# Kernel tuning notes

Hardware: AMD Instinct MI355X
Metric: run time of the kernel (lower is better)

Reference implementation:

```python
import jax, jax.numpy as jnp
import numpy as np

B, S, H = 2, 256, 768
LR = 0.01
EPS = 1e-5  # torch LayerNorm default


def setup_inputs() -> dict:
    key = jax.random.key(0)
    ks = jax.random.split(key, 6)
    f = jnp.float32
    return {
        "x": jax.random.normal(ks[0], (B, S, H), f),
        "W_init": jax.random.normal(ks[1], (H, H), f) * 0.02,
        "b_init": jnp.zeros((H,), f),
        "gate_w": jax.random.normal(ks[2], (4 * H, H), f) * 0.02,
        "gate_b": jnp.zeros((4 * H,), f),
        "up_w": jax.random.normal(ks[3], (4 * H, H), f) * 0.02,
        "up_b": jnp.zeros((4 * H,), f),
        "down_w": jax.random.normal(ks[4], (H, 4 * H), f) * 0.02,
        "down_b": jnp.zeros((H,), f),
        "norm_w": jnp.ones((H,), f),
        "norm_b": jnp.zeros((H,), f),
    }


def _layernorm(x, w, b):
    mu = jnp.mean(x, axis=-1, keepdims=True)
    var = jnp.var(x, axis=-1, keepdims=True)
    return (x - mu) * jax.lax.rsqrt(var + EPS) * w + b


def reference(x, W_init, b_init, gate_w, gate_b, up_w, up_b,
              down_w, down_b, norm_w, norm_b):
    # x: [B, S, H]. Sequential TTT fast-weight recurrence, vectorized over batch,
    # scanned over time (equivalent to the per-token Python loop in torch).
    Bn, Sn, Hn = x.shape
    xs = jnp.swapaxes(x, 0, 1)                                   # [S, B, H]
    x_next = jnp.concatenate([xs[1:], jnp.zeros_like(xs[:1])], 0)  # target x[t+1]
    # lr per step; the update is skipped at the last token (t == S-1)
    lr = jnp.concatenate([jnp.full((Sn - 1,), LR, x.dtype),
                          jnp.zeros((1,), x.dtype)])

    W0 = jnp.broadcast_to(W_init, (Bn, Hn, Hn))
    b0 = jnp.broadcast_to(b_init, (Bn, Hn))

    def step(carry, inp):
        W, b = carry
        xt, xn, lr_t = inp
        pred = jnp.einsum('bij,bj->bi', W, xt) + b               # fast-weight matvec
        gated = jax.nn.sigmoid(pred @ gate_w.T + gate_b) * (pred @ up_w.T + up_b)
        out = _layernorm(gated @ down_w.T + down_b + pred, norm_w, norm_b)
        diff = pred - xn                                         # prediction error
        W = W - lr_t * diff[:, :, None] * xt[:, None, :]         # rank-1 update
        b = b - lr_t * diff
        return (W, b), out

    _, ys = jax.lax.scan(step, (W0, b0), (xs, x_next, lr))       # ys: [S, B, H]
    return jnp.swapaxes(ys, 0, 1)
```

## Files before the change

kernel.cpp:

```cpp
#include <hip/hip_runtime.h>
#include <hip/hip_bf16.h>

#define H   768
#define H4  3072
#define S   256
#define BB  2
#define M   (BB * S)
#define LRC 0.01f
#define C   64
#define NC  (S / C)

typedef __attribute__((ext_vector_type(8))) short bf16x8;
typedef __attribute__((ext_vector_type(4))) float f32x4;

__device__ inline short bfbits(float f) {
    __hip_bfloat16 h = __float2bfloat16(f);
    return *reinterpret_cast<short*>(&h);
}

__global__ __launch_bounds__(256) void k_stage(
    const float* __restrict__ x,  const float* __restrict__ W0,
    const float* __restrict__ gw, const float* __restrict__ uw,
    const float* __restrict__ dw,
    short* __restrict__ Xhi, short* __restrict__ Xlo,
    short* __restrict__ Whi, short* __restrict__ Wlo,
    short* __restrict__ gw2, short* __restrict__ uw2, short* __restrict__ dw2)
{
    const long gid = (long)blockIdx.x * 256 + threadIdx.x;
    const float* src; short* hp; short* lp = nullptr; long base;
    if (gid < 98304)        { src = x;  hp = Xhi; lp = Xlo; base = 0; }
    else if (gid < 245760)  { src = W0; hp = Whi; lp = Wlo; base = 98304; }
    else if (gid < 835584)  { src = gw; hp = gw2; base = 245760; }
    else if (gid < 1425408) { src = uw; hp = uw2; base = 835584; }
    else                    { src = dw; hp = dw2; base = 1425408; }
    const long i = (gid - base) * 4;
    const float4 v = *(const float4*)(src + i);
    const float vf[4] = {v.x, v.y, v.z, v.w};
    short h4[4], l4[4];
#pragma unroll
    for (int j = 0; j < 4; ++j) {
        h4[j] = bfbits(vf[j]);
        __hip_bfloat16 hb = *reinterpret_cast<__hip_bfloat16*>(&h4[j]);
        l4[j] = bfbits(vf[j] - __bfloat162float(hb));
    }
    *(uint2*)(hp + i) = *(uint2*)h4;
    if (lp) *(uint2*)(lp + i) = *(uint2*)l4;
}

__global__ __launch_bounds__(256) void k_gram_base(
    const short* __restrict__ Xhi, const short* __restrict__ Xlo,
    const short* __restrict__ Whi, const short* __restrict__ Wlo,
    const float* __restrict__ b0,
    float* __restrict__ g, float* __restrict__ base0)
{
    const int wid = threadIdx.x >> 6, lane = threadIdx.x & 63;
    const int r16 = lane & 15, quad = lane >> 4;
    const int id = blockIdx.x;

    f32x4 acc[4];
#pragma unroll
    for (int i = 0; i < 4; ++i) acc[i] = (f32x4){0, 0, 0, 0};

    if (id < 32) {
        const int bx = id & 3, by = (id >> 2) & 3, b = id >> 4;
        const int m0 = by * 64, n0 = bx * 64 + wid * 16;
        const short* XH = Xhi + b * S * H;
        const short* XL = Xlo + b * S * H;
        for (int k0 = 0; k0 < H; k0 += 32) {
            const int k = k0 + quad * 8;
            const bf16x8 bh = *(const bf16x8*)(XH + (n0 + r16) * H + k);
            const bf16x8 bl = *(const bf16x8*)(XL + (n0 + r16) * H + k);
#pragma unroll
            for (int i = 0; i < 4; ++i) {
                const bf16x8 ah = *(const bf16x8*)(XH + (m0 + i * 16 + r16) * H + k);
                const bf16x8 al = *(const bf16x8*)(XL + (m0 + i * 16 + r16) * H + k);
                acc[i] = __builtin_amdgcn_mfma_f32_16x16x32_bf16(ah, bh, acc[i], 0, 0, 0);
                acc[i] = __builtin_amdgcn_mfma_f32_16x16x32_bf16(ah, bl, acc[i], 0, 0, 0);
                acc[i] = __builtin_amdgcn_mfma_f32_16x16x32_bf16(al, bh, acc[i], 0, 0, 0);
            }
        }
        const int col = n0 + r16;
#pragma unroll
        for (int i = 0; i < 4; ++i)
#pragma unroll
            for (int r = 0; r < 4; ++r) {
                const int row = m0 + i * 16 + quad * 4 + r;
                g[(b * S + row) * S + col] = acc[i][r] + 1.f;
            }
    } else {
        const int id2 = id - 32;
        const int m0 = (id2 / 12) * 64, n0 = (id2 % 12) * 64 + wid * 16;
        for (int k0 = 0; k0 < H; k0 += 32) {
            const int k = k0 + quad * 8;
            const bf16x8 bh = *(const bf16x8*)(Whi + (n0 + r16) * H + k);
            const bf16x8 bl = *(const bf16x8*)(Wlo + (n0 + r16) * H + k);
#pragma unroll
            for (int i = 0; i < 4; ++i) {
                const bf16x8 ah = *(const bf16x8*)(Xhi + (m0 + i * 16 + r16) * H + k);
                const bf16x8 al = *(const bf16x8*)(Xlo + (m0 + i * 16 + r16) * H + k);
                acc[i] = __builtin_amdgcn_mfma_f32_16x16x32_bf16(ah, bh, acc[i], 0, 0, 0);
                acc[i] = __builtin_amdgcn_mfma_f32_16x16x32_bf16(ah, bl, acc[i], 0, 0, 0);
                acc[i] = __builtin_amdgcn_mfma_f32_16x16x32_bf16(al, bh, acc[i], 0, 0, 0);
            }
        }
        const int col = n0 + r16;
        const float bv = b0[col];
#pragma unroll
        for (int i = 0; i < 4; ++i)
#pragma unroll
            for (int r = 0; r < 4; ++r) {
                const int row = m0 + i * 16 + quad * 4 + r;
                base0[row * H + col] = acc[i][r] + bv;
            }
    }
}

__global__ __launch_bounds__(256) void k_recur3(
    const float* __restrict__ x,
    const float* __restrict__ base0,
    const float* __restrict__ g,
    float* __restrict__ pred_f,
    __hip_bfloat16* __restrict__ pred_h)
{
    __shared__ float tB[64 * 17];
    __shared__ float tX[64 * 17];
    __shared__ float Dl[256 * 17];
    __shared__ float Gs[64 * 65];
    const int tid = threadIdx.x;
    const int w = tid >> 6, lane = tid & 63;
    const int b = blockIdx.x / 48, hb = blockIdx.x % 48;
    const int h0 = hb * 16;
    const int ho = w * 4;
    const int ct = tid >> 2;
    const int cq = (tid & 3) * 4;

    for (int c = 0; c < NC; ++c) {
        const int t0 = c * C;
        __syncthreads();
        {
            const int gm = b * S + t0 + ct;
            const float4 bv = *(const float4*)(base0 + gm * H + h0 + cq);
            float4 xv = {0.f, 0.f, 0.f, 0.f};
            if (t0 + ct + 1 < S)
                xv = *(const float4*)(x + (gm + 1) * H + h0 + cq);
            tB[ct * 17 + cq + 0] = bv.x - xv.x;
            tB[ct * 17 + cq + 1] = bv.y - xv.y;
            tB[ct * 17 + cq + 2] = bv.z - xv.z;
            tB[ct * 17 + cq + 3] = bv.w - xv.w;
            tX[ct * 17 + cq + 0] = xv.x;
            tX[ct * 17 + cq + 1] = xv.y;
            tX[ct * 17 + cq + 2] = xv.z;
            tX[ct * 17 + cq + 3] = xv.w;
#pragma unroll
            for (int j = 0; j < 16; ++j) {
                const int idx = tid + 256 * j;
                const int row = idx >> 6, col = idx & 63;
                Gs[row * 65 + col] = g[(long)(b * S + t0 + row) * S + t0 + col];
            }
        }
        __syncthreads();
        float R[4], Xn[4];
#pragma unroll
        for (int h = 0; h < 4; ++h) {
            R[h]  = tB[lane * 17 + ho + h];
            Xn[h] = tX[lane * 17 + ho + h];
        }
        const float* gcol = g + (long)(b * S) * S + t0 + lane;
#pragma unroll 4
        for (int cs = 0; cs < t0; ++cs) {
            const float Gv = gcol[(long)cs * S];
            const float* dr = &Dl[cs * 17 + ho];
            R[0] -= LRC * Gv * dr[0];
            R[1] -= LRC * Gv * dr[1];
            R[2] -= LRC * Gv * dr[2];
            R[3] -= LRC * Gv * dr[3];
        }
        for (int s = 0; s < C; ++s) {
            float dsb[4];
#pragma unroll
            for (int h = 0; h < 4; ++h) dsb[h] = __shfl(R[h], s, 64);
            const float Gv = Gs[s * 65 + lane];
            const float mlt = (lane > s) ? LRC : 0.f;
#pragma unroll
            for (int h = 0; h < 4; ++h) R[h] -= mlt * Gv * dsb[h];
        }
#pragma unroll
        for (int h = 0; h < 4; ++h) Dl[(t0 + lane) * 17 + ho + h] = R[h];
        __syncthreads();
#pragma unroll
        for (int h = 0; h < 4; ++h) tB[lane * 17 + ho + h] = R[h] + Xn[h];
        __syncthreads();
        {
            const int gm = b * S + t0 + ct;
            float4 pv;
            pv.x = tB[ct * 17 + cq + 0];
            pv.y = tB[ct * 17 + cq + 1];
            pv.z = tB[ct * 17 + cq + 2];
            pv.w = tB[ct * 17 + cq + 3];
            *(float4*)(pred_f + gm * H + h0 + cq) = pv;
            short p4[4];
            p4[0] = bfbits(pv.x); p4[1] = bfbits(pv.y);
            p4[2] = bfbits(pv.z); p4[3] = bfbits(pv.w);
            *(uint2*)((short*)pred_h + gm * H + h0 + cq) = *(uint2*)p4;
        }
    }
}

#define RS 40
__global__ __launch_bounds__(256) void k_gateup3(
    const __hip_bfloat16* __restrict__ predh,
    const short* __restrict__ gwp, const float* __restrict__ gb,
    const short* __restrict__ uwp, const float* __restrict__ ub,
    __hip_bfloat16* __restrict__ hid)
{
    __shared__ int4 smv[1600];
    short* sm = (short*)smv;
    short* sA = sm;
    short* sG = sm + 64 * RS;
    short* sU = sm + (64 + 128) * RS;

    const int tid = threadIdx.x;
    const int wid = tid >> 6, lane = tid & 63;
    const int r16 = lane & 15, quad = lane >> 4;
    const int wm = wid & 1, wn = wid >> 1;
    const int n0 = blockIdx.x * 128;
    const int m0 = blockIdx.y * 64;

    const int srow = tid >> 2;
    const int sch  = (tid & 3) * 8;
    const short* A = (const short*)predh;

    f32x4 ag[2][4], au[2][4];
#pragma unroll
    for (int i = 0; i < 2; ++i)
#pragma unroll
        for (int j = 0; j < 4; ++j) { ag[i][j] = (f32x4){0,0,0,0}; au[i][j] = (f32x4){0,0,0,0}; }

    int4 rA, rG0, rG1, rU0, rU1;
    {
        const int k = sch;
        rA  = *(const int4*)(A   + (m0 + srow) * H + k);
        rG0 = *(const int4*)(gwp + (n0 + srow) * H + k);
        rG1 = *(const int4*)(gwp + (n0 + 64 + srow) * H + k);
        rU0 = *(const int4*)(uwp + (n0 + srow) * H + k);
        rU1 = *(const int4*)(uwp + (n0 + 64 + srow) * H + k);
    }
    for (int it = 0; it < 24; ++it) {
        *(int4*)(sA + srow * RS + sch)        = rA;
        *(int4*)(sG + srow * RS + sch)        = rG0;
        *(int4*)(sG + (64 + srow) * RS + sch) = rG1;
        *(int4*)(sU + srow * RS + sch)        = rU0;
        *(int4*)(sU + (64 + srow) * RS + sch) = rU1;
        __syncthreads();
        if (it < 23) {
            const int k = (it + 1) * 32 + sch;
            rA  = *(const int4*)(A   + (m0 + srow) * H + k);
            rG0 = *(const int4*)(gwp + (n0 + srow) * H + k);
            rG1 = *(const int4*)(gwp + (n0 + 64 + srow) * H + k);
            rU0 = *(const int4*)(uwp + (n0 + srow) * H + k);
            rU1 = *(const int4*)(uwp + (n0 + 64 + srow) * H + k);
        }
        bf16x8 aF[2], gF[4], uF[4];
#pragma unroll
        for (int i = 0; i < 2; ++i)
            aF[i] = *(const bf16x8*)(sA + (wm * 32 + i * 16 + r16) * RS + quad * 8);
#pragma unroll
        for (int j = 0; j < 4; ++j) {
            gF[j] = *(const bf16x8*)(sG + (wn * 64 + j * 16 + r16) * RS + quad * 8);
            uF[j] = *(const bf16x8*)(sU + (wn * 64 + j * 16 + r16) * RS + quad * 8);
        }
#pragma unroll
        for (int i = 0; i < 2; ++i)
#pragma unroll
            for (int j = 0; j < 4; ++j) {
                ag[i][j] = __builtin_amdgcn_mfma_f32_16x16x32_bf16(aF[i], gF[j], ag[i][j], 0, 0, 0);
                au[i][j] = __builtin_amdgcn_mfma_f32_16x16x32_bf16(aF[i], uF[j], au[i][j], 0, 0, 0);
            }
        __syncthreads();
    }
#pragma unroll
    for (int j = 0; j < 4; ++j) {
        const int ocol = n0 + wn * 64 + j * 16 + r16;
        const float gbv = gb[ocol], ubv = ub[ocol];
#pragma unroll
        for (int i = 0; i < 2; ++i)
#pragma unroll
            for (int r = 0; r < 4; ++r) {
                const int orow = m0 + wm * 32 + i * 16 + quad * 4 + r;
                const float gg = ag[i][j][r] + gbv;
                const float u  = au[i][j][r] + ubv;
                const float sg = 1.f / (1.f + __expf(-gg));
                hid[orow * H4 + ocol] = __float2bfloat16(sg * u);
            }
    }
}

__device__ inline bf16x8 ldb32(const void* p, long off) {
    const float* f = (const float*)p + off;
    const float4 a = *(const float4*)f;
    const float4 b = *(const float4*)(f + 4);
    bf16x8 r;
    r[0] = bfbits(a.x); r[1] = bfbits(a.y); r[2] = bfbits(a.z); r[3] = bfbits(a.w);
    r[4] = bfbits(b.x); r[5] = bfbits(b.y); r[6] = bfbits(b.z); r[7] = bfbits(b.w);
    return r;
}
__device__ inline bf16x8 ldb16(const void* p, long off) {
    return *(const bf16x8*)((const short*)p + off);
}

template<bool WB>
__global__ __launch_bounds__(256) void k_gateup2(
    const __hip_bfloat16* __restrict__ predh,
    const void* __restrict__ gw, const float* __restrict__ gb,
    const void* __restrict__ uw, const float* __restrict__ ub,
    __hip_bfloat16* __restrict__ hid)
{
    const int wid = threadIdx.x >> 6, lane = threadIdx.x & 63;
    const int r16 = lane & 15, quad = lane >> 4;
    const int m0 = blockIdx.y * 64;
    const int n0 = blockIdx.x * 64 + wid * 16;

    f32x4 ag[4], au[4];
#pragma unroll
    for (int i = 0; i < 4; ++i) { ag[i] = (f32x4){0,0,0,0}; au[i] = (f32x4){0,0,0,0}; }
    const short* A = (const short*)predh;
    const long brow = (long)(n0 + r16) * H;

    for (int k0 = 0; k0 < H; k0 += 32) {
        const int k = k0 + quad * 8;
        const bf16x8 bg = WB ? ldb16(gw, brow + k) : ldb32(gw, brow + k);
        const bf16x8 bu = WB ? ldb16(uw, brow + k) : ldb32(uw, brow + k);
#pragma unroll
        for (int i = 0; i < 4; ++i) {
            const bf16x8 af = *(const bf16x8*)(A + (m0 + i * 16 + r16) * H + k);
            ag[i] = __builtin_amdgcn_mfma_f32_16x16x32_bf16(af, bg, ag[i], 0, 0, 0);
            au[i] = __builtin_amdgcn_mfma_f32_16x16x32_bf16(af, bu, au[i], 0, 0, 0);
        }
    }
    const int ocol = n0 + r16;
    const float gbv = gb[ocol], ubv = ub[ocol];
#pragma unroll
    for (int i = 0; i < 4; ++i)
#pragma unroll
        for (int r = 0; r < 4; ++r) {
            const int orow = m0 + i * 16 + quad * 4 + r;
            const float gg = ag[i][r] + gbv;
            const float u = au[i][r] + ubv;
            const float sg = 1.f / (1.f + __expf(-gg));
            hid[orow * H4 + ocol] = __float2bfloat16(sg * u);
        }
}

template<bool WB>
__global__ __launch_bounds__(256) void k_down2(
    const __hip_bfloat16* __restrict__ hid,
    const void* __restrict__ dw, const float* __restrict__ db,
    const float* __restrict__ predf, float* __restrict__ dout)
{
    const int wid = threadIdx.x >> 6, lane = threadIdx.x & 63;
    const int r16 = lane & 15, quad = lane >> 4;
    const int m0 = blockIdx.y * 32;
    const int n0 = blockIdx.x * 64 + wid * 16;

    f32x4 ac[2];
    ac[0] = (f32x4){0,0,0,0}; ac[1] = (f32x4){0,0,0,0};
    const short* A = (const short*)hid;
    const long brow = (long)(n0 + r16) * H4;

    for (int k0 = 0; k0 < H4; k0 += 32) {
        const int k = k0 + quad * 8;
        const bf16x8 bd = WB ? ldb16(dw, brow + k) : ldb32(dw, brow + k);
#pragma unroll
        for (int i = 0; i < 2; ++i) {
            const bf16x8 af = *(const bf16x8*)(A + (m0 + i * 16 + r16) * H4 + k);
            ac[i] = __builtin_amdgcn_mfma_f32_16x16x32_bf16(af, bd, ac[i], 0, 0, 0);
        }
    }
    const int ocol = n0 + r16;
    const float dbv = db[ocol];
#pragma unroll
    for (int i = 0; i < 2; ++i)
#pragma unroll
        for (int r = 0; r < 4; ++r) {
            const int orow = m0 + i * 16 + quad * 4 + r;
            dout[orow * H + ocol] = ac[i][r] + dbv + predf[orow * H + ocol];
        }
}

__global__ __launch_bounds__(256) void k_ln(
    const float* __restrict__ dout,
    const float* __restrict__ nw,
    const float* __restrict__ nb,
    float* __restrict__ out)
{
    const int m = blockIdx.x;
    const int tid = threadIdx.x;
    const float* rowp = dout + m * H;

    float v[3];
    float s = 0.f, s2 = 0.f;
#pragma unroll
    for (int j = 0; j < 3; ++j) {
        v[j] = rowp[tid + 256 * j];
        s += v[j];
        s2 += v[j] * v[j];
    }
#pragma unroll
    for (int off = 32; off >= 1; off >>= 1) {
        s  += __shfl_xor(s, off, 64);
        s2 += __shfl_xor(s2, off, 64);
    }
    __shared__ float rs[4], rs2[4];
    const int wid = tid >> 6, lane = tid & 63;
    if (lane == 0) { rs[wid] = s; rs2[wid] = s2; }
    __syncthreads();
    s  = rs[0] + rs[1] + rs[2] + rs[3];
    s2 = rs2[0] + rs2[1] + rs2[2] + rs2[3];
    const float mu  = s / (float)H;
    const float var = s2 / (float)H - mu * mu;
    const float inv = rsqrtf(var + 1e-5f);
#pragma unroll
    for (int j = 0; j < 3; ++j) {
        const int hh = tid + 256 * j;
        out[m * H + hh] = (v[j] - mu) * inv * nw[hh] + nb[hh];
    }
}

extern "C" void kernel_launch(void* const* d_in, const int* in_sizes, int n_in,
                              void* d_out, int out_size, void* d_ws, size_t ws_size,
                              hipStream_t stream)
{
    const float* x   = (const float*)d_in[0];
    const float* W0  = (const float*)d_in[1];
    const float* b0  = (const float*)d_in[2];
    const float* gw  = (const float*)d_in[3];
    const float* gb  = (const float*)d_in[4];
    const float* uw  = (const float*)d_in[5];
    const float* ub  = (const float*)d_in[6];
    const float* dw  = (const float*)d_in[7];
    const float* db  = (const float*)d_in[8];
    const float* nw  = (const float*)d_in[9];
    const float* nb  = (const float*)d_in[10];

    char* ws = (char*)d_ws;
    float*          pred_f = (float*)(ws);
    __hip_bfloat16* pred_h = (__hip_bfloat16*)(ws + 1572864);
    __hip_bfloat16* hid    = (__hip_bfloat16*)(ws + 2359296);
    float*          base0  = (float*)(ws + 5505024);
    float*          dout_f = (float*)(ws + 5505024);
    float*          g      = (float*)(ws + 7077888);
    short*          Xhi    = (short*)(ws + 7602176);
    short*          Xlo    = (short*)(ws + 8388608);
    short*          Whi    = (short*)(ws + 9175040);
    short*          Wlo    = (short*)(ws + 10354688);
    const size_t WNEED = 11534336ULL + 3ULL * 4718592ULL;
    const bool wb = ws_size >= WNEED;
    short* gw2 = (short*)(ws + 11534336);
    short* uw2 = (short*)(ws + 11534336 + 4718592);
    short* dw2 = (short*)(ws + 11534336 + 2 * 4718592);

    const int ngroups = wb ? 2015232 : 245760;
    k_stage<<<dim3(ngroups / 256), 256, 0, stream>>>(
        x, W0, gw, uw, dw, Xhi, Xlo, Whi, Wlo, gw2, uw2, dw2);
    k_gram_base<<<dim3(128), 256, 0, stream>>>(Xhi, Xlo, Whi, Wlo, b0, g, base0);
    k_recur3<<<dim3(96), 256, 0, stream>>>(x, base0, g, pred_f, pred_h);
    if (wb) {
        k_gateup3<<<dim3(H4 / 128, M / 64), 256, 0, stream>>>(pred_h, gw2, gb, uw2, ub, hid);
        k_down2<true><<<dim3(H / 64, M / 32), 256, 0, stream>>>(hid, dw2, db, pred_f, dout_f);
    } else {
        k_gateup2<false><<<dim3(H4 / 64, M / 64), 256, 0, stream>>>(pred_h, gw, gb, uw, ub, hid);
        k_down2<false><<<dim3(H / 64, M / 32), 256, 0, stream>>>(hid, dw, db, pred_f, dout_f);
    }
    k_ln<<<dim3(M), 256, 0, stream>>>(dout_f, nw, nb, (float*)d_out);
}
```

Baseline: 227.3 us.

## Fuse all stages into one cooperative persistent megakernel with grid syncs

Replaces the six separate kernel launches with a single cooperative kernel of 256 workgroups. The stages (weight staging, Gram/base GEMMs, recurrence, gate/up, down, layernorm) run in sequence, separated by grid.sync(). It also adds a precomputed per-chunk intra-chunk solve matrix U, computed in parallel, and re-splits the recurrence across 192 workgroups instead of 96. The aim is to remove launch gaps and raise parallelism in the serial recurrence. In exchange it adds grid-wide barrier costs, limits occupancy to one block per CU, and drops the fallback path for a small workspace.

```diff
diff --git a/kernel.cpp b/kernel.cpp
--- a/kernel.cpp
+++ b/kernel.cpp
@@ -1,5 +1,8 @@
 #include <hip/hip_runtime.h>
 #include <hip/hip_bf16.h>
+#include <hip/hip_cooperative_groups.h>
+
+namespace cg = cooperative_groups;
 
 #define H   768
 #define H4  3072
@@ -9,6 +12,8 @@
 #define LRC 0.01f
 #define C   64
 #define NC  (S / C)
+#define RS  40
+#define RS2 72
 
 typedef __attribute__((ext_vector_type(8))) short bf16x8;
 typedef __attribute__((ext_vector_type(4))) float f32x4;
@@ -18,411 +23,385 @@
     return *reinterpret_cast<short*>(&h);
 }
 
-__global__ __launch_bounds__(256) void k_stage(
+struct RecSM {
+    float2 Dl2[1024];
+    float2 Rl2[256];
+    float  tB[576];
+    float  tX[576];
+    float  Us[4160];
+    float  Gslab[12288];
+};
+union alignas(16) SM {
+    RecSM rec;
+    struct { short sA[64 * RS]; short sG[128 * RS]; short sU[128 * RS]; } gu;
+    struct { short sA[32 * RS2]; short sB[64 * RS2]; } dn;
+    float Gi[4160];
+    struct { float rs[4]; float rs2[4]; } ln;
+};
+
+__global__ void __launch_bounds__(256, 1) k_mega(
     const float* __restrict__ x,  const float* __restrict__ W0,
-    const float* __restrict__ gw, const float* __restrict__ uw,
-    const float* __restrict__ dw,
+    const float* __restrict__ b0,
+    const float* __restrict__ gw, const float* __restrict__ gb,
+    const float* __restrict__ uw, const float* __restrict__ ub,
+    const float* __restrict__ dw, const float* __restrict__ db,
+    const float* __restrict__ nw, const float* __restrict__ nb,
     short* __restrict__ Xhi, short* __restrict__ Xlo,
     short* __restrict__ Whi, short* __restrict__ Wlo,
-    short* __restrict__ gw2, short* __restrict__ uw2, short* __restrict__ dw2)
+    short* __restrict__ gw2, short* __restrict__ uw2, short* __restrict__ dw2,
+    float* __restrict__ g, float* __restrict__ base0, float* __restrict__ U,
+    float* __restrict__ pred_f, __hip_bfloat16* __restrict__ pred_h,
+    __hip_bfloat16* __restrict__ hid,
+    float* __restrict__ dout_f, float* __restrict__ out)
 {
-    const long gid = (long)blockIdx.x * 256 + threadIdx.x;
-    const float* src; short* hp; short* lp = nullptr; long base;
-    if (gid < 98304)        { src = x;  hp = Xhi; lp = Xlo; base = 0; }
-    else if (gid < 245760)  { src = W0; hp = Whi; lp = Wlo; base = 98304; }
-    else if (gid < 835584)  { src = gw; hp = gw2; base = 245760; }
-    else if (gid < 1425408) { src = uw; hp = uw2; base = 835584; }
-    else                    { src = dw; hp = dw2; base = 1425408; }
-    const long i = (gid - base) * 4;
-    const float4 v = *(const float4*)(src + i);
-    const float vf[4] = {v.x, v.y, v.z, v.w};
-    short h4[4], l4[4];
-#pragma unroll
-    for (int j = 0; j < 4; ++j) {
-        h4[j] = bfbits(vf[j]);
-        __hip_bfloat16 hb = *reinterpret_cast<__hip_bfloat16*>(&h4[j]);
-        l4[j] = bfbits(vf[j] - __bfloat162float(hb));
-    }
-    *(uint2*)(hp + i) = *(uint2*)h4;
-    if (lp) *(uint2*)(lp + i) = *(uint2*)l4;
-}
-
-__global__ __launch_bounds__(256) void k_gram_base(
-    const short* __restrict__ Xhi, const short* __restrict__ Xlo,
-    const short* __restrict__ Whi, const short* __restrict__ Wlo,
-    const float* __restrict__ b0,
-    float* __restrict__ g, float* __restrict__ base0)
-{
-    const int wid = threadIdx.x >> 6, lane = threadIdx.x & 63;
-    const int r16 = lane & 15, quad = lane >> 4;
-    const int id = blockIdx.x;
-
-    f32x4 acc[4];
-#pragma unroll
-    for (int i = 0; i < 4; ++i) acc[i] = (f32x4){0, 0, 0, 0};
-
-    if (id < 32) {
-        const int bx = id & 3, by = (id >> 2) & 3, b = id >> 4;
-        const int m0 = by * 64, n0 = bx * 64 + wid * 16;
-        const short* XH = Xhi + b * S * H;
-        const short* XL = Xlo + b * S * H;
-        for (int k0 = 0; k0 < H; k0 += 32) {
-            const int k = k0 + quad * 8;
-            const bf16x8 bh = *(const bf16x8*)(XH + (n0 + r16) * H + k);
-            const bf16x8 bl = *(const bf16x8*)(XL + (n0 + r16) * H + k);
-#pragma unroll
-            for (int i = 0; i < 4; ++i) {
-                const bf16x8 ah = *(const bf16x8*)(XH + (m0 + i * 16 + r16) * H + k);
-                const bf16x8 al = *(const bf16x8*)(XL + (m0 + i * 16 + r16) * H + k);
-                acc[i] = __builtin_amdgcn_mfma_f32_16x16x32_bf16(ah, bh, acc[i], 0, 0, 0);
-                acc[i] = __builtin_amdgcn_mfma_f32_16x16x32_bf16(ah, bl, acc[i], 0, 0, 0);
-                acc[i] = __builtin_amdgcn_mfma_f32_16x16x32_bf16(al, bh, acc[i], 0, 0, 0);
-            }
-        }
-        const int col = n0 + r16;
-#pragma unroll
-        for (int i = 0; i < 4; ++i)
-#pragma unroll
-            for (int r = 0; r < 4; ++r) {
-                const int row = m0 + i * 16 + quad * 4 + r;
-                g[(b * S + row) * S + col] = acc[i][r] + 1.f;
-            }
-    } else {
-        const int id2 = id - 32;
-        const int m0 = (id2 / 12) * 64, n0 = (id2 % 12) * 64 + wid * 16;
-        for (int k0 = 0; k0 < H; k0 += 32) {
-            const int k = k0 + quad * 8;
-            const bf16x8 bh = *(const bf16x8*)(Whi + (n0 + r16) * H + k);
-            const bf16x8 bl = *(const bf16x8*)(Wlo + (n0 + r16) * H + k);
-#pragma unroll
-            for (int i = 0; i < 4; ++i) {
-                const bf16x8 ah = *(const bf16x8*)(Xhi + (m0 + i * 16 + r16) * H + k);
-                const bf16x8 al = *(const bf16x8*)(Xlo + (m0 + i * 16 + r16) * H + k);
-                acc[i] = __builtin_amdgcn_mfma_f32_16x16x32_bf16(ah, bh, acc[i], 0, 0, 0);
-                acc[i] = __builtin_amdgcn_mfma_f32_16x16x32_bf16(ah, bl, acc[i], 0, 0, 0);
-                acc[i] = __builtin_amdgcn_mfma_f32_16x16x32_bf16(al, bh, acc[i], 0, 0, 0);
-            }
-        }
-        const int col = n0 + r16;
-        const float bv = b0[col];
-#pragma unroll
-        for (int i = 0; i < 4; ++i)
-#pragma unroll
-            for (int r = 0; r < 4; ++r) {
-                const int row = m0 + i * 16 + quad * 4 + r;
-                base0[row * H + col] = acc[i][r] + bv;
-            }
-    }
-}
-
-__global__ __launch_bounds__(256) void k_recur3(
-    const float* __restrict__ x,
-    const float* __restrict__ base0,
-    const float* __restrict__ g,
-    float* __restrict__ pred_f,
-    __hip_bfloat16* __restrict__ pred_h)
-{
-    __shared__ float tB[64 * 17];
-    __shared__ float tX[64 * 17];
-    __shared__ float Dl[256 * 17];
-    __shared__ float Gs[64 * 65];
+    __shared__ SM sm;
+    cg::grid_group grid = cg::this_grid();
     const int tid = threadIdx.x;
-    const int w = tid >> 6, lane = tid & 63;
-    const int b = blockIdx.x / 48, hb = blockIdx.x % 48;
-    const int h0 = hb * 16;
-    const int ho = w * 4;
-    const int ct = tid >> 2;
-    const int cq = (tid & 3) * 4;
-
-    for (int c = 0; c < NC; ++c) {
-        const int t0 = c * C;
-        __syncthreads();
-        {
-            const int gm = b * S + t0 + ct;
-            const float4 bv = *(const float4*)(base0 + gm * H + h0 + cq);
-            float4 xv = {0.f, 0.f, 0.f, 0.f};
-            if (t0 + ct + 1 < S)
-                xv = *(const float4*)(x + (gm + 1) * H + h0 + cq);
-            tB[ct * 17 + cq + 0] = bv.x - xv.x;
-            tB[ct * 17 + cq + 1] = bv.y - xv.y;
-            tB[ct * 17 + cq + 2] = bv.z - xv.z;
-            tB[ct * 17 + cq + 3] = bv.w - xv.w;
-            tX[ct * 17 + cq + 0] = xv.x;
-            tX[ct * 17 + cq + 1] = xv.y;
-            tX[ct * 17 + cq + 2] = xv.z;
-            tX[ct * 17 + cq + 3] = xv.w;
-#pragma unroll
-            for (int j = 0; j < 16; ++j) {
-                const int idx = tid + 256 * j;
-                const int row = idx >> 6, col = idx & 63;
-                Gs[row * 65 + col] = g[(long)(b * S + t0 + row) * S + t0 + col];
-            }
-        }
-        __syncthreads();
-        float R[4], Xn[4];
-#pragma unroll
-        for (int h = 0; h < 4; ++h) {
-            R[h]  = tB[lane * 17 + ho + h];
-            Xn[h] = tX[lane * 17 + ho + h];
-        }
-        const float* gcol = g + (long)(b * S) * S + t0 + lane;
-#pragma unroll 4
-        for (int cs = 0; cs < t0; ++cs) {
-            const float Gv = gcol[(long)cs * S];
-            const float* dr = &Dl[cs * 17 + ho];
-            R[0] -= LRC * Gv * dr[0];
-            R[1] -= LRC * Gv * dr[1];
-            R[2] -= LRC * Gv * dr[2];
-            R[3] -= LRC * Gv * dr[3];
-        }
-        for (int s = 0; s < C; ++s) {
-            float dsb[4];
-#pragma unroll
-            for (int h = 0; h < 4; ++h) dsb[h] = __shfl(R[h], s, 64);
-            const float Gv = Gs[s * 65 + lane];
-            const float mlt = (lane > s) ? LRC : 0.f;
-#pragma unroll
-            for (int h = 0; h < 4; ++h) R[h] -= mlt * Gv * dsb[h];
-        }
-#pragma unroll
-        for (int h = 0; h < 4; ++h) Dl[(t0 + lane) * 17 + ho + h] = R[h];
-        __syncthreads();
-#pragma unroll
-        for (int h = 0; h < 4; ++h) tB[lane * 17 + ho + h] = R[h] + Xn[h];
-        __syncthreads();
-        {
-            const int gm = b * S + t0 + ct;
-            float4 pv;
-            pv.x = tB[ct * 17 + cq + 0];
-            pv.y = tB[ct * 17 + cq + 1];
-            pv.z = tB[ct * 17 + cq + 2];
-            pv.w = tB[ct * 17 + cq + 3];
-            *(float4*)(pred_f + gm * H + h0 + cq) = pv;
-            short p4[4];
-            p4[0] = bfbits(pv.x); p4[1] = bfbits(pv.y);
-            p4[2] = bfbits(pv.z); p4[3] = bfbits(pv.w);
-            *(uint2*)((short*)pred_h + gm * H + h0 + cq) = *(uint2*)p4;
-        }
-    }
-}
-
-#define RS 40
-__global__ __launch_bounds__(256) void k_gateup3(
-    const __hip_bfloat16* __restrict__ predh,
-    const short* __restrict__ gwp, const float* __restrict__ gb,
-    const short* __restrict__ uwp, const float* __restrict__ ub,
-    __hip_bfloat16* __restrict__ hid)
-{
-    __shared__ int4 smv[1600];
-    short* sm = (short*)smv;
-    short* sA = sm;
-    short* sG = sm + 64 * RS;
-    short* sU = sm + (64 + 128) * RS;
-
-    const int tid = threadIdx.x;
+    const int wg  = blockIdx.x;
     const int wid = tid >> 6, lane = tid & 63;
     const int r16 = lane & 15, quad = lane >> 4;
-    const int wm = wid & 1, wn = wid >> 1;
-    const int n0 = blockIdx.x * 128;
-    const int m0 = blockIdx.y * 64;
-
-    const int srow = tid >> 2;
-    const int sch  = (tid & 3) * 8;
-    const short* A = (const short*)predh;
-
-    f32x4 ag[2][4], au[2][4];
-#pragma unroll
-    for (int i = 0; i < 2; ++i)
-#pragma unroll
-        for (int j = 0; j < 4; ++j) { ag[i][j] = (f32x4){0,0,0,0}; au[i][j] = (f32x4){0,0,0,0}; }
-
-    int4 rA, rG0, rG1, rU0, rU1;
+
+    for (long gid = (long)wg * 256 + tid; gid < 2015232; gid += 65536) {
+        const float* src; short* hp; short* lp = nullptr; long base;
+        if (gid < 98304)        { src = x;  hp = Xhi; lp = Xlo; base = 0; }
+        else if (gid < 245760)  { src = W0; hp = Whi; lp = Wlo; base = 98304; }
+        else if (gid < 835584)  { src = gw; hp = gw2; base = 245760; }
+        else if (gid < 1425408) { src = uw; hp = uw2; base = 835584; }
+        else                    { src = dw; hp = dw2; base = 1425408; }
+        const long i = (gid - base) * 4;
+        const float4 v = *(const float4*)(src + i);
+        const float vf[4] = {v.x, v.y, v.z, v.w};
+        short h4[4], l4[4];
+#pragma unroll
+        for (int j = 0; j < 4; ++j) {
+            h4[j] = bfbits(vf[j]);
+            __hip_bfloat16 hb = *reinterpret_cast<__hip_bfloat16*>(&h4[j]);
+            l4[j] = bfbits(vf[j] - __bfloat162float(hb));
+        }
+        *(uint2*)(hp + i) = *(uint2*)h4;
+        if (lp) *(uint2*)(lp + i) = *(uint2*)l4;
+    }
+    grid.sync();
+
     {
-        const int k = sch;
-        rA  = *(const int4*)(A   + (m0 + srow) * H + k);
-        rG0 = *(const int4*)(gwp + (n0 + srow) * H + k);
-        rG1 = *(const int4*)(gwp + (n0 + 64 + srow) * H + k);
-        rU0 = *(const int4*)(uwp + (n0 + srow) * H + k);
-        rU1 = *(const int4*)(uwp + (n0 + 64 + srow) * H + k);
-    }
-    for (int it = 0; it < 24; ++it) {
-        *(int4*)(sA + srow * RS + sch)        = rA;
-        *(int4*)(sG + srow * RS + sch)        = rG0;
-        *(int4*)(sG + (64 + srow) * RS + sch) = rG1;
-        *(int4*)(sU + srow * RS + sch)        = rU0;
-        *(int4*)(sU + (64 + srow) * RS + sch) = rU1;
+        f32x4 acc[2];
+        acc[0] = (f32x4){0, 0, 0, 0};
+        acc[1] = (f32x4){0, 0, 0, 0};
+        if (wg < 64) {
+            const int bx = wg & 3, by = (wg >> 2) & 7, b = wg >> 5;
+            const int m0 = by * 32, n0 = bx * 64 + wid * 16;
+            const short* XH = Xhi + b * S * H;
+            const short* XL = Xlo + b * S * H;
+            for (int k0 = 0; k0 < H; k0 += 32) {
+                const int k = k0 + quad * 8;
+                const bf16x8 bh = *(const bf16x8*)(XH + (n0 + r16) * H + k);
+                const bf16x8 bl = *(const bf16x8*)(XL + (n0 + r16) * H + k);
+#pragma unroll
+                for (int i = 0; i < 2; ++i) {
+                    const bf16x8 ah = *(const bf16x8*)(XH + (m0 + i * 16 + r16) * H + k);
+                    const bf16x8 al = *(const bf16x8*)(XL + (m0 + i * 16 + r16) * H + k);
+                    acc[i] = __builtin_amdgcn_mfma_f32_16x16x32_bf16(ah, bh, acc[i], 0, 0, 0);
+                    acc[i] = __builtin_amdgcn_mfma_f32_16x16x32_bf16(ah, bl, acc[i], 0, 0, 0);
+                    acc[i] = __builtin_amdgcn_mfma_f32_16x16x32_bf16(al, bh, acc[i], 0, 0, 0);
+                }
+            }
+            const int col = n0 + r16;
+#pragma unroll
+            for (int i = 0; i < 2; ++i)
+#pragma unroll
+                for (int r = 0; r < 4; ++r) {
+                    const int row = m0 + i * 16 + quad * 4 + r;
+                    g[(b * S + row) * S + col] = acc[i][r] + 1.f;
+                }
+        } else {
+            const int id2 = wg - 64;
+            const int m0 = (id2 / 12) * 32, n0 = (id2 % 12) * 64 + wid * 16;
+            for (int k0 = 0; k0 < H; k0 += 32) {
+                const int k = k0 + quad * 8;
+                const bf16x8 bh = *(const bf16x8*)(Whi + (n0 + r16) * H + k);
+                const bf16x8 bl = *(const bf16x8*)(Wlo + (n0 + r16) * H + k);
+#pragma unroll
+                for (int i = 0; i < 2; ++i) {
+                    const bf16x8 ah = *(const bf16x8*)(Xhi + (m0 + i * 16 + r16) * H + k);
+                    const bf16x8 al = *(const bf16x8*)(Xlo + (m0 + i * 16 + r16) * H + k);
+                    acc[i] = __builtin_amdgcn_mfma_f32_16x16x32_bf16(ah, bh, acc[i], 0, 0, 0);
+                    acc[i] = __builtin_amdgcn_mfma_f32_16x16x32_bf16(ah, bl, acc[i], 0, 0, 0);
+                    acc[i] = __builtin_amdgcn_mfma_f32_16x16x32_bf16(al, bh, acc[i], 0, 0, 0);
+                }
+            }
+            const int col = n0 + r16;
+            const float bv = b0[col];
+#pragma unroll
+            for (int i = 0; i < 2; ++i)
+#pragma unroll
+                for (int r = 0; r < 4; ++r) {
+                    const int row = m0 + i * 16 + quad * 4 + r;
+                    base0[row * H + col] = acc[i][r] + bv;
+                }
+        }
+    }
+    grid.sync();
+
+    if (wg < BB * NC) {
+        const int b = wg >> 2, c = wg & 3;
+        const int t0 = c * C;
+#pragma unroll
+        for (int j = 0; j < 16; ++j) {
+            const int idx = tid + 256 * j;
+            const int row = idx >> 6, col = idx & 63;
+            sm.Gi[row * 65 + col] = g[(long)(b * S + t0 + row) * S + t0 + col];
+        }
         __syncthreads();
-        if (it < 23) {
-            const int k = (it + 1) * 32 + sch;
-            rA  = *(const int4*)(A   + (m0 + srow) * H + k);
-            rG0 = *(const int4*)(gwp + (n0 + srow) * H + k);
-            rG1 = *(const int4*)(gwp + (n0 + 64 + srow) * H + k);
-            rU0 = *(const int4*)(uwp + (n0 + srow) * H + k);
-            rU1 = *(const int4*)(uwp + (n0 + 64 + srow) * H + k);
-        }
-        bf16x8 aF[2], gF[4], uF[4];
+        const int j0 = wid * 16;
+        float R[16];
+#pragma unroll
+        for (int i = 0; i < 16; ++i) R[i] = (lane == j0 + i) ? 1.f : 0.f;
+        for (int s = 0; s < C - 1; ++s) {
+            const float Gv = sm.Gi[s * 65 + lane];
+            const float mlt = (lane > s) ? LRC : 0.f;
+#pragma unroll
+            for (int i = 0; i < 16; ++i) {
+                const float dsb = __shfl(R[i], s, 64);
+                R[i] -= mlt * Gv * dsb;
+            }
+        }
+        float* Ub = U + (long)(b * NC + c) * C * C;
+#pragma unroll
+        for (int i = 0; i < 16; ++i)
+            Ub[lane * C + j0 + i] = R[i];
+    }
+    grid.sync();
+
+    if (wg < 192) {
+        const int b = wg / 96, hb = wg % 96;
+        const int h0 = hb * 8;
+        const int ho = wid * 2;
+        const int ct = tid >> 2;
+        const int cq = (tid & 3) * 2;
+        for (int c = 0; c < NC; ++c) {
+            const int t0 = c * C;
+            __syncthreads();
+            {
+                const int gm = b * S + t0 + ct;
+                const float2 bv = *(const float2*)(base0 + gm * H + h0 + cq);
+                float2 xv = {0.f, 0.f};
+                if (t0 + ct + 1 < S)
+                    xv = *(const float2*)(x + (gm + 1) * H + h0 + cq);
+                sm.rec.tB[ct * 9 + cq + 0] = bv.x - xv.x;
+                sm.rec.tB[ct * 9 + cq + 1] = bv.y - xv.y;
+                sm.rec.tX[ct * 9 + cq + 0] = xv.x;
+                sm.rec.tX[ct * 9 + cq + 1] = xv.y;
+                const float* Ub = U + (long)(b * NC + c) * C * C;
+#pragma unroll
+                for (int j = 0; j < 16; ++j) {
+                    const int idx = tid + 256 * j;
+                    const int row = idx >> 6, col = idx & 63;
+                    sm.rec.Us[row * 65 + col] = Ub[row * C + col];
+                }
+                const float* gb2 = g + (long)(b * S) * S + t0;
+                for (int i = tid; i < t0 * 64; i += 256) {
+                    const int row = i >> 6, col = i & 63;
+                    sm.rec.Gslab[i] = gb2[(long)row * S + col];
+                }
+            }
+            __syncthreads();
+            float R[2], Xn[2];
+#pragma unroll
+            for (int h = 0; h < 2; ++h) {
+                R[h]  = sm.rec.tB[lane * 9 + ho + h];
+                Xn[h] = sm.rec.tX[lane * 9 + ho + h];
+            }
+#pragma unroll 8
+            for (int cs = 0; cs < t0; ++cs) {
+                const float Gv = sm.rec.Gslab[cs * 64 + lane];
+                const float2 dr = sm.rec.Dl2[cs * 4 + wid];
+                R[0] -= LRC * Gv * dr.x;
+                R[1] -= LRC * Gv * dr.y;
+            }
+            sm.rec.Rl2[wid * 64 + lane] = (float2){R[0], R[1]};
+            float D[2] = {0.f, 0.f};
+#pragma unroll 8
+            for (int s = 0; s < C; ++s) {
+                const float2 rb = sm.rec.Rl2[wid * 64 + s];
+                const float uv = sm.rec.Us[lane * 65 + s];
+                D[0] += uv * rb.x;
+                D[1] += uv * rb.y;
+            }
+            sm.rec.Dl2[(t0 + lane) * 4 + wid] = (float2){D[0], D[1]};
+            __syncthreads();
+#pragma unroll
+            for (int h = 0; h < 2; ++h) sm.rec.tB[lane * 9 + ho + h] = D[h] + Xn[h];
+            __syncthreads();
+            {
+                const int gm = b * S + t0 + ct;
+                float2 pv;
+                pv.x = sm.rec.tB[ct * 9 + cq + 0];
+                pv.y = sm.rec.tB[ct * 9 + cq + 1];
+                *(float2*)(pred_f + gm * H + h0 + cq) = pv;
+                short p2[2];
+                p2[0] = bfbits(pv.x); p2[1] = bfbits(pv.y);
+                *(unsigned int*)((short*)pred_h + gm * H + h0 + cq) = *(unsigned int*)p2;
+            }
+        }
+    }
+    grid.sync();
+
+    if (wg < 192) {
+        const int n0 = (wg % 24) * 128;
+        const int m0 = (wg / 24) * 64;
+        const int wm = wid & 1, wn = wid >> 1;
+        const int srow = tid >> 2;
+        const int sch  = (tid & 3) * 8;
+        const short* A = (const short*)pred_h;
+
+        f32x4 ag[2][4], au[2][4];
 #pragma unroll
         for (int i = 0; i < 2; ++i)
-            aF[i] = *(const bf16x8*)(sA + (wm * 32 + i * 16 + r16) * RS + quad * 8);
+#pragma unroll
+            for (int j = 0; j < 4; ++j) { ag[i][j] = (f32x4){0,0,0,0}; au[i][j] = (f32x4){0,0,0,0}; }
+
+        int4 rA, rG0, rG1, rU0, rU1;
+        rA  = *(const int4*)(A   + (m0 + srow) * H + sch);
+        rG0 = *(const int4*)(gw2 + (n0 + srow) * H + sch);
+        rG1 = *(const int4*)(gw2 + (n0 + 64 + srow) * H + sch);
+        rU0 = *(const int4*)(uw2 + (n0 + srow) * H + sch);
+        rU1 = *(const int4*)(uw2 + (n0 + 64 + srow) * H + sch);
+        for (int it = 0; it < 24; ++it) {
+            *(int4*)(sm.gu.sA + srow * RS + sch)        = rA;
+            *(int4*)(sm.gu.sG + srow * RS + sch)        = rG0;
+            *(int4*)(sm.gu.sG + (64 + srow) * RS + sch) = rG1;
+            *(int4*)(sm.gu.sU + srow * RS + sch)        = rU0;
+            *(int4*)(sm.gu.sU + (64 + srow) * RS + sch) = rU1;
+            __syncthreads();
+            if (it < 23) {
+                const int k = (it + 1) * 32 + sch;
+                rA  = *(const int4*)(A   + (m0 + srow) * H + k);
+                rG0 = *(const int4*)(gw2 + (n0 + srow) * H + k);
+                rG1 = *(const int4*)(gw2 + (n0 + 64 + srow) * H + k);
+                rU0 = *(const int4*)(uw2 + (n0 + srow) * H + k);
+                rU1 = *(const int4*)(uw2 + (n0 + 64 + srow) * H + k);
+            }
+            bf16x8 aF[2], gF[4], uF[4];
+#pragma unroll
+            for (int i = 0; i < 2; ++i)
+                aF[i] = *(const bf16x8*)(sm.gu.sA + (wm * 32 + i * 16 + r16) * RS + quad * 8);
+#pragma unroll
+            for (int j = 0; j < 4; ++j) {
+                gF[j] = *(const bf16x8*)(sm.gu.sG + (wn * 64 + j * 16 + r16) * RS + quad * 8);
+                uF[j] = *(const bf16x8*)(sm.gu.sU + (wn * 64 + j * 16 + r16) * RS + quad * 8);
+            }
+#pragma unroll
+            for (int i = 0; i < 2; ++i)
+#pragma unroll
+                for (int j = 0; j < 4; ++j) {
+                    ag[i][j] = __builtin_amdgcn_mfma_f32_16x16x32_bf16(aF[i], gF[j], ag[i][j], 0, 0, 0);
+                    au[i][j] = __builtin_amdgcn_mfma_f32_16x16x32_bf16(aF[i], uF[j], au[i][j], 0, 0, 0);
+                }
+            __syncthreads();
+        }
 #pragma unroll
         for (int j = 0; j < 4; ++j) {
-            gF[j] = *(const bf16x8*)(sG + (wn * 64 + j * 16 + r16) * RS + quad * 8);
-            uF[j] = *(const bf16x8*)(sU + (wn * 64 + j * 16 + r16) * RS + quad * 8);
-        }
-#pragma unroll
-        for (int i = 0; i < 2; ++i)
-#pragma unroll
-            for (int j = 0; j < 4; ++j) {
-                ag[i][j] = __builtin_amdgcn_mfma_f32_16x16x32_bf16(aF[i], gF[j], ag[i][j], 0, 0, 0);
-                au[i][j] = __builtin_amdgcn_mfma_f32_16x16x32_bf16(aF[i], uF[j], au[i][j], 0, 0, 0);
-            }
+            const int ocol = n0 + wn * 64 + j * 16 + r16;
+            const float gbv = gb[ocol], ubv = ub[ocol];
+#pragma unroll
+            for (int i = 0; i < 2; ++i)
+#pragma unroll
+                for (int r = 0; r < 4; ++r) {
+                    const int orow = m0 + wm * 32 + i * 16 + quad * 4 + r;
+                    const float gg = ag[i][j][r] + gbv;
+                    const float u  = au[i][j][r] + ubv;
+                    const float sg = 1.f / (1.f + __expf(-gg));
+                    hid[orow * H4 + ocol] = __float2bfloat16(sg * u);
+                }
+        }
+    }
+    grid.sync();
+
+    if (wg < 192) {
+        const int n0 = (wg % 12) * 64;
+        const int m0 = (wg / 12) * 32;
+        const int wm = wid & 1, wn = wid >> 1;
+        const short* A = (const short*)hid;
+
+        f32x4 ac[2];
+        ac[0] = (f32x4){0,0,0,0}; ac[1] = (f32x4){0,0,0,0};
+
+        const int arow = tid >> 3, ach = (tid & 7) * 8;
+        const int brow1 = arow + 32;
+
+        int4 rA, rB0, rB1;
+        rA  = *(const int4*)(A   + (m0 + arow) * H4 + ach);
+        rB0 = *(const int4*)(dw2 + (n0 + arow) * H4 + ach);
+        rB1 = *(const int4*)(dw2 + (n0 + brow1) * H4 + ach);
+        for (int it = 0; it < 48; ++it) {
+            *(int4*)(sm.dn.sA + arow * RS2 + ach)  = rA;
+            *(int4*)(sm.dn.sB + arow * RS2 + ach)  = rB0;
+            *(int4*)(sm.dn.sB + brow1 * RS2 + ach) = rB1;
+            __syncthreads();
+            if (it < 47) {
+                const int k = (it + 1) * 64 + ach;
+                rA  = *(const int4*)(A   + (m0 + arow) * H4 + k);
+                rB0 = *(const int4*)(dw2 + (n0 + arow) * H4 + k);
+                rB1 = *(const int4*)(dw2 + (n0 + brow1) * H4 + k);
+            }
+            bf16x8 aF[2], bF[2][2];
+#pragma unroll
+            for (int kk = 0; kk < 2; ++kk) {
+                aF[kk] = *(const bf16x8*)(sm.dn.sA + (wm * 16 + r16) * RS2 + kk * 32 + quad * 8);
+#pragma unroll
+                for (int j = 0; j < 2; ++j)
+                    bF[j][kk] = *(const bf16x8*)(sm.dn.sB + (wn * 32 + j * 16 + r16) * RS2 + kk * 32 + quad * 8);
+            }
+#pragma unroll
+            for (int kk = 0; kk < 2; ++kk)
+#pragma unroll
+                for (int j = 0; j < 2; ++j)
+                    ac[j] = __builtin_amdgcn_mfma_f32_16x16x32_bf16(aF[kk], bF[j][kk], ac[j], 0, 0, 0);
+            __syncthreads();
+        }
+#pragma unroll
+        for (int j = 0; j < 2; ++j) {
+            const int ocol = n0 + wn * 32 + j * 16 + r16;
+            const float dbv = db[ocol];
+#pragma unroll
+            for (int r = 0; r < 4; ++r) {
+                const int orow = m0 + wm * 16 + quad * 4 + r;
+                dout_f[orow * H + ocol] = ac[j][r] + dbv + pred_f[orow * H + ocol];
+            }
+        }
+    }
+    grid.sync();
+
+    for (int rr = 0; rr < 2; ++rr) {
+        const int m = wg * 2 + rr;
+        const float* rowp = dout_f + m * H;
+        float v[3];
+        float s = 0.f, s2 = 0.f;
+#pragma unroll
+        for (int j = 0; j < 3; ++j) {
+            v[j] = rowp[tid + 256 * j];
+            s += v[j];
+            s2 += v[j] * v[j];
+        }
+#pragma unroll
+        for (int off = 32; off >= 1; off >>= 1) {
+            s  += __shfl_xor(s, off, 64);
+            s2 += __shfl_xor(s2, off, 64);
+        }
         __syncthreads();
-    }
-#pragma unroll
-    for (int j = 0; j < 4; ++j) {
-        const int ocol = n0 + wn * 64 + j * 16 + r16;
-        const float gbv = gb[ocol], ubv = ub[ocol];
-#pragma unroll
-        for (int i = 0; i < 2; ++i)
-#pragma unroll
-            for (int r = 0; r < 4; ++r) {
-                const int orow = m0 + wm * 32 + i * 16 + quad * 4 + r;
-                const float gg = ag[i][j][r] + gbv;
-                const float u  = au[i][j][r] + ubv;
-                const float sg = 1.f / (1.f + __expf(-gg));
-                hid[orow * H4 + ocol] = __float2bfloat16(sg * u);
-            }
-    }
-}
-
-__device__ inline bf16x8 ldb32(const void* p, long off) {
-    const float* f = (const float*)p + off;
-    const float4 a = *(const float4*)f;
-    const float4 b = *(const float4*)(f + 4);
-    bf16x8 r;
-    r[0] = bfbits(a.x); r[1] = bfbits(a.y); r[2] = bfbits(a.z); r[3] = bfbits(a.w);
-    r[4] = bfbits(b.x); r[5] = bfbits(b.y); r[6] = bfbits(b.z); r[7] = bfbits(b.w);
-    return r;
-}
-__device__ inline bf16x8 ldb16(const void* p, long off) {
-    return *(const bf16x8*)((const short*)p + off);
-}
-
-template<bool WB>
-__global__ __launch_bounds__(256) void k_gateup2(
-    const __hip_bfloat16* __restrict__ predh,
-    const void* __restrict__ gw, const float* __restrict__ gb,
-    const void* __restrict__ uw, const float* __restrict__ ub,
-    __hip_bfloat16* __restrict__ hid)
-{
-    const int wid = threadIdx.x >> 6, lane = threadIdx.x & 63;
-    const int r16 = lane & 15, quad = lane >> 4;
-    const int m0 = blockIdx.y * 64;
-    const int n0 = blockIdx.x * 64 + wid * 16;
-
-    f32x4 ag[4], au[4];
-#pragma unroll
-    for (int i = 0; i < 4; ++i) { ag[i] = (f32x4){0,0,0,0}; au[i] = (f32x4){0,0,0,0}; }
-    const short* A = (const short*)predh;
-    const long brow = (long)(n0 + r16) * H;
-
-    for (int k0 = 0; k0 < H; k0 += 32) {
-        const int k = k0 + quad * 8;
-        const bf16x8 bg = WB ? ldb16(gw, brow + k) : ldb32(gw, brow + k);
-        const bf16x8 bu = WB ? ldb16(uw, brow + k) : ldb32(uw, brow + k);
-#pragma unroll
-        for (int i = 0; i < 4; ++i) {
-            const bf16x8 af = *(const bf16x8*)(A + (m0 + i * 16 + r16) * H + k);
-            ag[i] = __builtin_amdgcn_mfma_f32_16x16x32_bf16(af, bg, ag[i], 0, 0, 0);
-            au[i] = __builtin_amdgcn_mfma_f32_16x16x32_bf16(af, bu, au[i], 0, 0, 0);
-        }
-    }
-    const int ocol = n0 + r16;
-    const float gbv = gb[ocol], ubv = ub[ocol];
-#pragma unroll
-    for (int i = 0; i < 4; ++i)
-#pragma unroll
-        for (int r = 0; r < 4; ++r) {
-            const int orow = m0 + i * 16 + quad * 4 + r;
-            const float gg = ag[i][r] + gbv;
-            const float u = au[i][r] + ubv;
-            const float sg = 1.f / (1.f + __expf(-gg));
-            hid[orow * H4 + ocol] = __float2bfloat16(sg * u);
-        }
-}
-
-template<bool WB>
-__global__ __launch_bounds__(256) void k_down2(
-    const __hip_bfloat16* __restrict__ hid,
-    const void* __restrict__ dw, const float* __restrict__ db,
-    const float* __restrict__ predf, float* __restrict__ dout)
-{
-    const int wid = threadIdx.x >> 6, lane = threadIdx.x & 63;
-    const int r16 = lane & 15, quad = lane >> 4;
-    const int m0 = blockIdx.y * 32;
-    const int n0 = blockIdx.x * 64 + wid * 16;
-
-    f32x4 ac[2];
-    ac[0] = (f32x4){0,0,0,0}; ac[1] = (f32x4){0,0,0,0};
-    const short* A = (const short*)hid;
-    const long brow = (long)(n0 + r16) * H4;
-
-    for (int k0 = 0; k0 < H4; k0 += 32) {
-        const int k = k0 + quad * 8;
-        const bf16x8 bd = WB ? ldb16(dw, brow + k) : ldb32(dw, brow + k);
-#pragma unroll
-        for (int i = 0; i < 2; ++i) {
-            const bf16x8 af = *(const bf16x8*)(A + (m0 + i * 16 + r16) * H4 + k);
-            ac[i] = __builtin_amdgcn_mfma_f32_16x16x32_bf16(af, bd, ac[i], 0, 0, 0);
-        }
-    }
-    const int ocol = n0 + r16;
-    const float dbv = db[ocol];
-#pragma unroll
-    for (int i = 0; i < 2; ++i)
-#pragma unroll
-        for (int r = 0; r < 4; ++r) {
-            const int orow = m0 + i * 16 + quad * 4 + r;
-            dout[orow * H + ocol] = ac[i][r] + dbv + predf[orow * H + ocol];
-        }
-}
-
-__global__ __launch_bounds__(256) void k_ln(
-    const float* __restrict__ dout,
-    const float* __restrict__ nw,
-    const float* __restrict__ nb,
-    float* __restrict__ out)
-{
-    const int m = blockIdx.x;
-    const int tid = threadIdx.x;
-    const float* rowp = dout + m * H;
-
-    float v[3];
-    float s = 0.f, s2 = 0.f;
-#pragma unroll
-    for (int j = 0; j < 3; ++j) {
-        v[j] = rowp[tid + 256 * j];
-        s += v[j];
-        s2 += v[j] * v[j];
-    }
-#pragma unroll
-    for (int off = 32; off >= 1; off >>= 1) {
-        s  += __shfl_xor(s, off, 64);
-        s2 += __shfl_xor(s2, off, 64);
-    }
-    __shared__ float rs[4], rs2[4];
-    const int wid = tid >> 6, lane = tid & 63;
-    if (lane == 0) { rs[wid] = s; rs2[wid] = s2; }
-    __syncthreads();
-    s  = rs[0] + rs[1] + rs[2] + rs[3];
-    s2 = rs2[0] + rs2[1] + rs2[2] + rs2[3];
-    const float mu  = s / (float)H;
-    const float var = s2 / (float)H - mu * mu;
-    const float inv = rsqrtf(var + 1e-5f);
-#pragma unroll
-    for (int j = 0; j < 3; ++j) {
-        const int hh = tid + 256 * j;
-        out[m * H + hh] = (v[j] - mu) * inv * nw[hh] + nb[hh];
+        if (lane == 0) { sm.ln.rs[wid] = s; sm.ln.rs2[wid] = s2; }
+        __syncthreads();
+        s  = sm.ln.rs[0] + sm.ln.rs[1] + sm.ln.rs[2] + sm.ln.rs[3];
+        s2 = sm.ln.rs2[0] + sm.ln.rs2[1] + sm.ln.rs2[2] + sm.ln.rs2[3];
+        const float mu  = s / (float)H;
+        const float var = s2 / (float)H - mu * mu;
+        const float inv = rsqrtf(var + 1e-5f);
+#pragma unroll
+        for (int j = 0; j < 3; ++j) {
+            const int hh = tid + 256 * j;
+            out[m * H + hh] = (v[j] - mu) * inv * nw[hh] + nb[hh];
+        }
+        __syncthreads();
     }
 }
 
@@ -447,29 +426,27 @@
     __hip_bfloat16* pred_h = (__hip_bfloat16*)(ws + 1572864);
     __hip_bfloat16* hid    = (__hip_bfloat16*)(ws + 2359296);
     float*          base0  = (float*)(ws + 5505024);
-    float*          dout_f = (float*)(ws + 5505024);
     float*          g      = (float*)(ws + 7077888);
     short*          Xhi    = (short*)(ws + 7602176);
     short*          Xlo    = (short*)(ws + 8388608);
     short*          Whi    = (short*)(ws + 9175040);
     short*          Wlo    = (short*)(ws + 10354688);
-    const size_t WNEED = 11534336ULL + 3ULL * 4718592ULL;
-    const bool wb = ws_size >= WNEED;
-    short* gw2 = (short*)(ws + 11534336);
-    short* uw2 = (short*)(ws + 11534336 + 4718592);
-    short* dw2 = (short*)(ws + 11534336 + 2 * 4718592);
-
-    const int ngroups = wb ? 2015232 : 245760;
-    k_stage<<<dim3(ngroups / 256), 256, 0, stream>>>(
-        x, W0, gw, uw, dw, Xhi, Xlo, Whi, Wlo, gw2, uw2, dw2);
-    k_gram_base<<<dim3(128), 256, 0, stream>>>(Xhi, Xlo, Whi, Wlo, b0, g, base0);
-    k_recur3<<<dim3(96), 256, 0, stream>>>(x, base0, g, pred_f, pred_h);
-    if (wb) {
-        k_gateup3<<<dim3(H4 / 128, M / 64), 256, 0, stream>>>(pred_h, gw2, gb, uw2, ub, hid);
-        k_down2<true><<<dim3(H / 64, M / 32), 256, 0, stream>>>(hid, dw2, db, pred_f, dout_f);
-    } else {
-        k_gateup2<false><<<dim3(H4 / 64, M / 64), 256, 0, stream>>>(pred_h, gw, gb, uw, ub, hid);
-        k_down2<false><<<dim3(H / 64, M / 32), 256, 0, stream>>>(hid, dw, db, pred_f, dout_f);
-    }
-    k_ln<<<dim3(M), 256, 0, stream>>>(dout_f, nw, nb, (float*)d_out);
+    float*          U      = (float*)(ws + 11534336);
+    short*          gw2    = (short*)(ws + 11665408);
+    short*          uw2    = (short*)(ws + 11665408 + 4718592);
+    short*          dw2    = (short*)(ws + 11665408 + 2 * 4718592);
+    float*          dout_f = (float*)(ws + 25821184);
+    float*          out    = (float*)d_out;
+
+    void* args[] = {
+        (void*)&x, (void*)&W0, (void*)&b0, (void*)&gw, (void*)&gb,
+        (void*)&uw, (void*)&ub, (void*)&dw, (void*)&db, (void*)&nw, (void*)&nb,
+        (void*)&Xhi, (void*)&Xlo, (void*)&Whi, (void*)&Wlo,
+        (void*)&gw2, (void*)&uw2, (void*)&dw2,
+        (void*)&g, (void*)&base0, (void*)&U,
+        (void*)&pred_f, (void*)&pred_h, (void*)&hid,
+        (void*)&dout_f, (void*)&out
+    };
+    (void)hipLaunchCooperativeKernel((void*)k_mega, dim3(256), dim3(256),
+                                     args, 0, stream);
 }
```

New measurement: 382.6 us. 1.68x slower.
